# Kernel tuning notes

Measured on AMD Instinct MI355X. Metric: run time of the kernel, lower is better.

Reference implementation:

```python
import jax, jax.numpy as jnp
import numpy as np

B, T, C, H = 4, 4096, 1024, 64

def setup_inputs() -> dict:
    key = jax.random.key(0)
    kx, kk, kq, kv = jax.random.split(key, 4)
    x = jax.random.normal(kx, (B, T, C), dtype=jnp.float32)
    # causal lower-triangular mask; masked_fill where mask == 0
    mask = jnp.tril(jnp.ones((T, T), dtype=jnp.int32))
    s = 1.0 / np.sqrt(C)
    Wk = jax.random.normal(kk, (H, C), dtype=jnp.float32) * s
    Wq = jax.random.normal(kq, (H, C), dtype=jnp.float32) * s
    Wv = jax.random.normal(kv, (H, C), dtype=jnp.float32) * s
    return {"x": x, "mask": mask, "Wk": Wk, "Wq": Wq, "Wv": Wv}

def reference(x, mask, Wk, Wq, Wv):
    # single-head attention; dropout is identity in eval mode
    scale = Wk.shape[0] ** -0.5  # head_size ** -0.5
    k = jnp.einsum('btc,hc->bth', x, Wk)  # [B,T,H]
    q = jnp.einsum('btc,hc->bth', x, Wq)
    v = jnp.einsum('btc,hc->bth', x, Wv)
    att = jnp.einsum('bqh,bkh->bqk', q, k) * scale  # [B,T,T]
    att = jnp.where(mask == 0, -jnp.inf, att)
    att = jax.nn.softmax(att, axis=-1)
    out = jnp.einsum('bqk,bkh->bqh', att, v)  # [B,T,H]
    return out
```

## Files before the change

kernel.cpp:

```cpp
#include <hip/hip_runtime.h>
#include <hip/hip_bf16.h>

#define BT 16384
#define CDIM 1024
#define HD 64
#define TT 4096

typedef __bf16 bf16x8 __attribute__((ext_vector_type(8)));
typedef __bf16 bf16x4 __attribute__((ext_vector_type(4)));
typedef float f32x4 __attribute__((ext_vector_type(4)));

__device__ __forceinline__ f32x4 mfma16(bf16x8 a, bf16x8 b, f32x4 c){
  return __builtin_amdgcn_mfma_f32_16x16x32_bf16(a, b, c, 0, 0, 0);
}

__global__ __launch_bounds__(256) void wconv_k(const float* __restrict__ Wk,
    const float* __restrict__ Wq, const float* __restrict__ Wv,
    __bf16* __restrict__ Wbf){
  int idx = blockIdx.x*256 + threadIdx.x;
  int e0 = idx*4;
  int n = e0 >> 10;
  int c = e0 & 1023;
  const float* src; float s;
  if (n < 64)      { src = Wk + (size_t)n*CDIM;       s = 1.0f;   }
  else if (n < 128){ src = Wq + (size_t)(n-64)*CDIM;  s = 0.125f; }
  else             { src = Wv + (size_t)(n-128)*CDIM; s = 1.0f;   }
  float4 v = *reinterpret_cast<const float4*>(src + c);
  __bf16* dst = Wbf + e0;
  dst[0]=(__bf16)(v.x*s); dst[1]=(__bf16)(v.y*s);
  dst[2]=(__bf16)(v.z*s); dst[3]=(__bf16)(v.w*s);
}

__global__ __launch_bounds__(512) void proj_k(const float* __restrict__ x,
    const __bf16* __restrict__ Wbf, __bf16* __restrict__ kb,
    __bf16* __restrict__ qb, __bf16* __restrict__ vTb){
  __shared__ __bf16 Xall[32][1032];
  __shared__ __bf16 Wt[2][192][68];

  const int tid  = threadIdx.x;
  const int lane = tid & 63;
  const int w    = tid >> 6;
  const int wr   = w >> 2;
  const int wn   = w & 3;
  const int l15  = lane & 15, g = lane >> 4;
  const long row0 = (long)blockIdx.x*32;

  #pragma unroll
  for (int p=0; p<16; ++p){
    const int idx = p*512 + tid;
    const int rw  = idx >> 8;
    const int c4  = (idx & 255)*4;
    float4 v = *reinterpret_cast<const float4*>(x + (row0 + rw)*CDIM + c4);
    bf16x4 xv;
    xv[0]=(__bf16)v.x; xv[1]=(__bf16)v.y; xv[2]=(__bf16)v.z; xv[3]=(__bf16)v.w;
    *reinterpret_cast<bf16x4*>(&Xall[rw][c4]) = xv;
  }

  const int wrw0 = tid>>3, wrw1 = (tid+512)>>3, wrw2 = (tid+1024)>>3;
  const int wc8  = (tid & 7)*8;
  const __bf16* ws0 = Wbf + (size_t)wrw0*CDIM + wc8;
  const __bf16* ws1 = Wbf + (size_t)wrw1*CDIM + wc8;
  const __bf16* ws2 = Wbf + (size_t)wrw2*CDIM + wc8;

  f32x4 acc[3];
  #pragma unroll
  for (int j=0;j<3;j++) acc[j] = (f32x4)(0.0f);

  bf16x8 w0, w1, w2;

  w0 = *reinterpret_cast<const bf16x8*>(ws0);
  w1 = *reinterpret_cast<const bf16x8*>(ws1);
  w2 = *reinterpret_cast<const bf16x8*>(ws2);
  *reinterpret_cast<bf16x8*>(&Wt[0][wrw0][wc8]) = w0;
  *reinterpret_cast<bf16x8*>(&Wt[0][wrw1][wc8]) = w1;
  *reinterpret_cast<bf16x8*>(&Wt[0][wrw2][wc8]) = w2;
  w0 = *reinterpret_cast<const bf16x8*>(ws0 + 64);
  w1 = *reinterpret_cast<const bf16x8*>(ws1 + 64);
  w2 = *reinterpret_cast<const bf16x8*>(ws2 + 64);
  __syncthreads();

  #pragma unroll 2
  for (int t=0; t<16; ++t){
    const int cur = t & 1, nxt = cur ^ 1;

    if (t+1 < 16){
      *reinterpret_cast<bf16x8*>(&Wt[nxt][wrw0][wc8]) = w0;
      *reinterpret_cast<bf16x8*>(&Wt[nxt][wrw1][wc8]) = w1;
      *reinterpret_cast<bf16x8*>(&Wt[nxt][wrw2][wc8]) = w2;
    }
    if (t+2 < 16){
      const int nk0 = (t+2)*64;
      w0 = *reinterpret_cast<const bf16x8*>(ws0 + nk0);
      w1 = *reinterpret_cast<const bf16x8*>(ws1 + nk0);
      w2 = *reinterpret_cast<const bf16x8*>(ws2 + nk0);
    }
    {
      const int k0 = t*64;
      bf16x8 a0 = *reinterpret_cast<const bf16x8*>(&Xall[wr*16 + l15][k0 + g*8]);
      bf16x8 a1 = *reinterpret_cast<const bf16x8*>(&Xall[wr*16 + l15][k0 + g*8 + 32]);
      bf16x8 b0[3], b1[3];
      #pragma unroll
      for (int nf=0;nf<3;nf++){
        b0[nf] = *reinterpret_cast<const bf16x8*>(&Wt[cur][wn*48 + nf*16 + l15][g*8]);
        b1[nf] = *reinterpret_cast<const bf16x8*>(&Wt[cur][wn*48 + nf*16 + l15][g*8 + 32]);
      }
      #pragma unroll
      for (int nf=0;nf<3;nf++)
        acc[nf] = mfma16(a1, b1[nf], mfma16(a0, b0[nf], acc[nf]));
    }
    __syncthreads();
  }

  const long bidx = row0 >> 12;
  #pragma unroll
  for (int nf=0;nf<3;nf++){
    const int n0  = wn*48 + nf*16 + l15;
    const int mat = n0 >> 6;
    const int h   = n0 & 63;
    const long rbase = row0 + wr*16 + g*4;
    if (mat == 0){
      #pragma unroll
      for (int r=0;r<4;r++) kb[(rbase+r)*HD + h] = (__bf16)acc[nf][r];
    } else if (mat == 1){
      #pragma unroll
      for (int r=0;r<4;r++) qb[(rbase+r)*HD + h] = (__bf16)acc[nf][r];
    } else {
      bf16x4 t4;
      #pragma unroll
      for (int r=0;r<4;r++) t4[r] = (__bf16)acc[nf][r];
      *reinterpret_cast<bf16x4*>(vTb + (bidx*64 + h)*TT + (rbase & 4095)) = t4;
    }
  }
}

template<int NS>
__global__ __launch_bounds__(256) void attn_part_k(const __bf16* __restrict__ kbg,
    const __bf16* __restrict__ qbg, const __bf16* __restrict__ vT,
    __bf16* __restrict__ po, float* __restrict__ pl){
  __shared__ __bf16 Klds[64][68];
  __shared__ __bf16 Vlds[64][68];
  __shared__ __bf16 Plds[4][16][68];

  const int tid  = threadIdx.x;
  const int lane = tid & 63;
  const int w    = tid >> 6;
  const int l15  = lane & 15, g = lane >> 4;

  const int bi  = blockIdx.x;
  const int b   = bi / (64*NS);
  const int rem = bi % (64*NS);
  const int qt  = 63 - rem / NS;
  const int s   = rem % NS;

  const int ntiles = qt + 1;
  const int lo = ( s      * ntiles) / NS;
  const int hi = ((s + 1) * ntiles) / NS;
  const int pidx = (b*64 + qt)*NS + s;

  if (lo == hi){
    if (l15 == 0){
      #pragma unroll
      for (int r=0;r<4;r++) pl[pidx*64 + w*16 + g*4 + r] = 0.0f;
    }
    return;
  }

  const long qbase = (long)b*TT + (long)qt*64;

  bf16x8 qf0, qf1;
  {
    const __bf16* src = qbg + (qbase + w*16 + l15)*HD + g*8;
    qf0 = *reinterpret_cast<const bf16x8*>(src);
    qf1 = *reinterpret_cast<const bf16x8*>(src + 32);
  }

  f32x4 o[4];
  #pragma unroll
  for (int ch=0; ch<4; ++ch) o[ch] = (f32x4)(0.0f);
  float lp[4] = {0.f, 0.f, 0.f, 0.f};

  const __bf16* vbase = vT + (size_t)b*64*TT;

  const int skey = tid >> 2;
  const int sd0  = (tid & 3) * 16;
  bf16x8 kr0, kr1, vr0, vr1;

  {
    const long kvbase = (long)b*TT + (long)lo*64;
    const __bf16* ks = kbg + (kvbase + skey)*HD + sd0;
    kr0 = *reinterpret_cast<const bf16x8*>(ks);
    kr1 = *reinterpret_cast<const bf16x8*>(ks+8);
    const __bf16* vs = vbase + (size_t)skey*TT + lo*64 + sd0;
    vr0 = *reinterpret_cast<const bf16x8*>(vs);
    vr1 = *reinterpret_cast<const bf16x8*>(vs+8);
  }

  for (int kv=lo; kv<hi; ++kv){
    __syncthreads();
    *reinterpret_cast<bf16x8*>(&Klds[skey][sd0])   = kr0;
    *reinterpret_cast<bf16x8*>(&Klds[skey][sd0+8]) = kr1;
    *reinterpret_cast<bf16x8*>(&Vlds[skey][sd0])   = vr0;
    *reinterpret_cast<bf16x8*>(&Vlds[skey][sd0+8]) = vr1;
    __syncthreads();

    if (kv+1 < hi){
      const long nbase = (long)b*TT + (long)(kv+1)*64;
      const __bf16* ks = kbg + (nbase + skey)*HD + sd0;
      kr0 = *reinterpret_cast<const bf16x8*>(ks);
      kr1 = *reinterpret_cast<const bf16x8*>(ks+8);
      const __bf16* vs = vbase + (size_t)skey*TT + (kv+1)*64 + sd0;
      vr0 = *reinterpret_cast<const bf16x8*>(vs);
      vr1 = *reinterpret_cast<const bf16x8*>(vs+8);
    }

    f32x4 sv[4];
    __builtin_amdgcn_s_setprio(1);
    #pragma unroll
    for (int c=0;c<4;c++){
      bf16x8 kb0 = *reinterpret_cast<const bf16x8*>(&Klds[c*16 + l15][g*8]);
      bf16x8 kb1 = *reinterpret_cast<const bf16x8*>(&Klds[c*16 + l15][g*8 + 32]);
      sv[c] = mfma16(qf0, kb0, (f32x4)(-16.0f));
      sv[c] = mfma16(qf1, kb1, sv[c]);
    }
    __builtin_amdgcn_s_setprio(0);

    if (kv == qt){
      #pragma unroll
      for (int c=0;c<4;c++){
        const int key = c*16 + l15;
        #pragma unroll
        for (int r=0;r<4;r++){
          const int qr = w*16 + g*4 + r;
          if (key > qr) sv[c][r] = -1e30f;
        }
      }
    }

    #pragma unroll
    for (int c=0;c<4;c++){
      #pragma unroll
      for (int r=0;r<4;r++) sv[c][r] = __expf(sv[c][r]);
    }
    #pragma unroll
    for (int r=0;r<4;r++)
      lp[r] += (sv[0][r] + sv[1][r]) + (sv[2][r] + sv[3][r]);

    #pragma unroll
    for (int c=0;c<4;c++){
      #pragma unroll
      for (int r=0;r<4;r++) Plds[w][g*4+r][c*16 + l15] = (__bf16)sv[c][r];
    }
    asm volatile("s_waitcnt lgkmcnt(0)" ::: "memory");
    __builtin_amdgcn_sched_barrier(0);
    bf16x8 pa0 = *reinterpret_cast<const bf16x8*>(&Plds[w][l15][g*8]);
    bf16x8 pa1 = *reinterpret_cast<const bf16x8*>(&Plds[w][l15][g*8 + 32]);

    __builtin_amdgcn_s_setprio(1);
    #pragma unroll
    for (int ch=0; ch<4; ++ch){
      bf16x8 vb0 = *reinterpret_cast<const bf16x8*>(&Vlds[ch*16 + l15][g*8]);
      bf16x8 vb1 = *reinterpret_cast<const bf16x8*>(&Vlds[ch*16 + l15][g*8 + 32]);
      o[ch] = mfma16(pa0, vb0, o[ch]);
      o[ch] = mfma16(pa1, vb1, o[ch]);
    }
    __builtin_amdgcn_s_setprio(0);
  }

  float lr[4];
  #pragma unroll
  for (int r=0;r<4;r++){
    float v = lp[r];
    v += __shfl_xor(v, 1);
    v += __shfl_xor(v, 2);
    v += __shfl_xor(v, 4);
    v += __shfl_xor(v, 8);
    lr[r] = v;
  }
  float rl[4];
  #pragma unroll
  for (int r=0;r<4;r++) rl[r] = (lr[r] > 0.0f) ? 1.0f/lr[r] : 0.0f;

  __bf16* podst = po + (size_t)pidx*4096;
  #pragma unroll
  for (int ch=0; ch<4; ++ch){
    #pragma unroll
    for (int r=0;r<4;r++)
      podst[(w*16 + g*4 + r)*64 + ch*16 + l15] = (__bf16)(o[ch][r] * rl[r]);
  }
  if (l15 == 0){
    #pragma unroll
    for (int r=0;r<4;r++) pl[pidx*64 + w*16 + g*4 + r] = lr[r];
  }
}

template<int NS>
__global__ __launch_bounds__(256) void comb_k(const __bf16* __restrict__ po,
    const float* __restrict__ pl, float* __restrict__ out){
  const int idx   = blockIdx.x*256 + threadIdx.x;
  const int qrow  = idx >> 6;
  const int dim   = idx & 63;
  const int qtg   = qrow >> 6;
  const int rowin = qrow & 63;

  float num = 0.0f, den = 0.0f;
  #pragma unroll
  for (int s=0;s<NS;s++){
    const float l = pl[(qtg*NS + s)*64 + rowin];
    den += l;
    num += l * (float)po[(size_t)(qtg*NS + s)*4096 + rowin*64 + dim];
  }
  out[idx] = num / den;
}

extern "C" void kernel_launch(void* const* d_in, const int* in_sizes, int n_in,
                              void* d_out, int out_size, void* d_ws, size_t ws_size,
                              hipStream_t stream) {
  const float* x  = (const float*)d_in[0];
  const float* Wk = (const float*)d_in[2];
  const float* Wq = (const float*)d_in[3];
  const float* Wv = (const float*)d_in[4];
  float* out = (float*)d_out;

  char* ws = (char*)d_ws;
  __bf16* Wbf = (__bf16*)ws;
  __bf16* kb  = (__bf16*)(ws + 393216);
  __bf16* qb  = (__bf16*)(ws + 2490368);
  __bf16* vTb = (__bf16*)(ws + 4587520);
  __bf16* po  = (__bf16*)(ws + 6684672);

  wconv_k<<<192, 256, 0, stream>>>(Wk, Wq, Wv, Wbf);
  proj_k <<<512, 512, 0, stream>>>(x, Wbf, kb, qb, vTb);

  const size_t need8 = 6684672ull + (size_t)2048*4096*2 + (size_t)2048*64*4;
  if (ws_size >= need8){
    float* pl = (float*)(ws + 6684672 + (size_t)2048*4096*2);
    attn_part_k<8><<<2048, 256, 0, stream>>>(kb, qb, vTb, po, pl);
    comb_k<8>    <<<4096, 256, 0, stream>>>(po, pl, out);
  } else {
    float* pl = (float*)(ws + 6684672 + (size_t)1024*4096*2);
    attn_part_k<4><<<1024, 256, 0, stream>>>(kb, qb, vTb, po, pl);
    comb_k<4>    <<<4096, 256, 0, stream>>>(po, pl, out);
  }
}
```

Before: 68.96 us.

## Load projection weights directly from global memory and repad LDS arrays

The projection kernel stops staging the bf16 weight tiles through double-buffered shared memory. Each wave now reads its MFMA B fragments straight from global memory (L2/L1-cached), which removes the per-iteration barrier and the LDS writes. The X buffer row padding changes from 1032 to 1048, and the attention kernel's LDS row pitch changes from 68 to 72, altering bank-conflict patterns and alignment. The trade-off is that weight fragments are no longer shared through LDS, so redundant global loads and exposed latency may increase without prefetching.

```diff
diff --git a/kernel.cpp b/kernel.cpp
--- a/kernel.cpp
+++ b/kernel.cpp
@@ -34,8 +34,7 @@
 __global__ __launch_bounds__(512) void proj_k(const float* __restrict__ x,
     const __bf16* __restrict__ Wbf, __bf16* __restrict__ kb,
     __bf16* __restrict__ qb, __bf16* __restrict__ vTb){
-  __shared__ __bf16 Xall[32][1032];
-  __shared__ __bf16 Wt[2][192][68];
+  __shared__ __bf16 Xall[32][1048];
 
   const int tid  = threadIdx.x;
   const int lane = tid & 63;
@@ -55,60 +54,31 @@
     xv[0]=(__bf16)v.x; xv[1]=(__bf16)v.y; xv[2]=(__bf16)v.z; xv[3]=(__bf16)v.w;
     *reinterpret_cast<bf16x4*>(&Xall[rw][c4]) = xv;
   }
-
-  const int wrw0 = tid>>3, wrw1 = (tid+512)>>3, wrw2 = (tid+1024)>>3;
-  const int wc8  = (tid & 7)*8;
-  const __bf16* ws0 = Wbf + (size_t)wrw0*CDIM + wc8;
-  const __bf16* ws1 = Wbf + (size_t)wrw1*CDIM + wc8;
-  const __bf16* ws2 = Wbf + (size_t)wrw2*CDIM + wc8;
+  __syncthreads();
 
   f32x4 acc[3];
   #pragma unroll
   for (int j=0;j<3;j++) acc[j] = (f32x4)(0.0f);
 
-  bf16x8 w0, w1, w2;
-
-  w0 = *reinterpret_cast<const bf16x8*>(ws0);
-  w1 = *reinterpret_cast<const bf16x8*>(ws1);
-  w2 = *reinterpret_cast<const bf16x8*>(ws2);
-  *reinterpret_cast<bf16x8*>(&Wt[0][wrw0][wc8]) = w0;
-  *reinterpret_cast<bf16x8*>(&Wt[0][wrw1][wc8]) = w1;
-  *reinterpret_cast<bf16x8*>(&Wt[0][wrw2][wc8]) = w2;
-  w0 = *reinterpret_cast<const bf16x8*>(ws0 + 64);
-  w1 = *reinterpret_cast<const bf16x8*>(ws1 + 64);
-  w2 = *reinterpret_cast<const bf16x8*>(ws2 + 64);
-  __syncthreads();
+  const __bf16* wb0 = Wbf + (size_t)(wn*48 +  0 + l15)*CDIM + g*8;
+  const __bf16* wb1 = Wbf + (size_t)(wn*48 + 16 + l15)*CDIM + g*8;
+  const __bf16* wb2 = Wbf + (size_t)(wn*48 + 32 + l15)*CDIM + g*8;
+  const __bf16* xrow = &Xall[wr*16 + l15][0];
 
   #pragma unroll 2
   for (int t=0; t<16; ++t){
-    const int cur = t & 1, nxt = cur ^ 1;
-
-    if (t+1 < 16){
-      *reinterpret_cast<bf16x8*>(&Wt[nxt][wrw0][wc8]) = w0;
-      *reinterpret_cast<bf16x8*>(&Wt[nxt][wrw1][wc8]) = w1;
-      *reinterpret_cast<bf16x8*>(&Wt[nxt][wrw2][wc8]) = w2;
-    }
-    if (t+2 < 16){
-      const int nk0 = (t+2)*64;
-      w0 = *reinterpret_cast<const bf16x8*>(ws0 + nk0);
-      w1 = *reinterpret_cast<const bf16x8*>(ws1 + nk0);
-      w2 = *reinterpret_cast<const bf16x8*>(ws2 + nk0);
-    }
-    {
-      const int k0 = t*64;
-      bf16x8 a0 = *reinterpret_cast<const bf16x8*>(&Xall[wr*16 + l15][k0 + g*8]);
-      bf16x8 a1 = *reinterpret_cast<const bf16x8*>(&Xall[wr*16 + l15][k0 + g*8 + 32]);
-      bf16x8 b0[3], b1[3];
-      #pragma unroll
-      for (int nf=0;nf<3;nf++){
-        b0[nf] = *reinterpret_cast<const bf16x8*>(&Wt[cur][wn*48 + nf*16 + l15][g*8]);
-        b1[nf] = *reinterpret_cast<const bf16x8*>(&Wt[cur][wn*48 + nf*16 + l15][g*8 + 32]);
-      }
-      #pragma unroll
-      for (int nf=0;nf<3;nf++)
-        acc[nf] = mfma16(a1, b1[nf], mfma16(a0, b0[nf], acc[nf]));
-    }
-    __syncthreads();
+    const int k0 = t*64;
+    bf16x8 a0 = *reinterpret_cast<const bf16x8*>(xrow + k0 + g*8);
+    bf16x8 a1 = *reinterpret_cast<const bf16x8*>(xrow + k0 + g*8 + 32);
+    bf16x8 b00 = *reinterpret_cast<const bf16x8*>(wb0 + k0);
+    bf16x8 b01 = *reinterpret_cast<const bf16x8*>(wb0 + k0 + 32);
+    bf16x8 b10 = *reinterpret_cast<const bf16x8*>(wb1 + k0);
+    bf16x8 b11 = *reinterpret_cast<const bf16x8*>(wb1 + k0 + 32);
+    bf16x8 b20 = *reinterpret_cast<const bf16x8*>(wb2 + k0);
+    bf16x8 b21 = *reinterpret_cast<const bf16x8*>(wb2 + k0 + 32);
+    acc[0] = mfma16(a1, b01, mfma16(a0, b00, acc[0]));
+    acc[1] = mfma16(a1, b11, mfma16(a0, b10, acc[1]));
+    acc[2] = mfma16(a1, b21, mfma16(a0, b20, acc[2]));
   }
 
   const long bidx = row0 >> 12;
@@ -137,9 +107,9 @@
 __global__ __launch_bounds__(256) void attn_part_k(const __bf16* __restrict__ kbg,
     const __bf16* __restrict__ qbg, const __bf16* __restrict__ vT,
     __bf16* __restrict__ po, float* __restrict__ pl){
-  __shared__ __bf16 Klds[64][68];
-  __shared__ __bf16 Vlds[64][68];
-  __shared__ __bf16 Plds[4][16][68];
+  __shared__ __bf16 Klds[64][72];
+  __shared__ __bf16 Vlds[64][72];
+  __shared__ __bf16 Plds[4][16][72];
 
   const int tid  = threadIdx.x;
   const int lane = tid & 63;
```

New measurement: 92.74 us. +34.5%, slower.
